# Kernel optimization log

Measured on AMD Instinct MI355X. Metric: run time of the kernel, lower is better.

Reference implementation:

```python
import jax, jax.numpy as jnp
import numpy as np

C = 64      # in_channels
H = 32      # hidden_size per direction
K = 8       # kernel_size
L = 4       # num_layers
EPS = 1e-5


def _sru_dir(x, W, v, b, reverse):
    # x: (T, N, in); one SRU direction.
    if reverse:
        x = x[::-1]
    U = x @ W                                   # (T, N, 4H): [candidate z, f_pre, r_pre, highway x']
    z, fp, rp, xp = jnp.split(U, 4, axis=-1)
    vf, vr = jnp.split(v, 2)
    bf, br = jnp.split(b, 2)

    def step(c, inp):
        z_t, fp_t, rp_t, xp_t = inp
        f = jax.nn.sigmoid(fp_t + vf * c + bf)
        r = jax.nn.sigmoid(rp_t + vr * c + br)
        c_new = f * c + (1.0 - f) * z_t
        h = r * c_new + (1.0 - r) * xp_t
        return c_new, h

    c0 = jnp.zeros((x.shape[1], H), x.dtype)
    _, h = jax.lax.scan(step, c0, (z, fp, rp, xp))
    if reverse:
        h = h[::-1]
    return h


def _sru(x, W0, Wr, v, b):
    # Bidirectional multi-layer SRU. x: (T, N, C*K) -> (T, N, 2H)
    Ws = [W0] + [Wr[i] for i in range(Wr.shape[0])]
    h = x
    for l in range(L):
        hf = _sru_dir(h, Ws[l][0], v[l, 0], b[l, 0], False)
        hb = _sru_dir(h, Ws[l][1], v[l, 1], b[l, 1], True)
        h = jnp.concatenate([hf, hb], axis=-1)
    return h


def setup_inputs() -> dict:
    key = jax.random.key(0)
    ks = jax.random.split(key, 8)
    B, Fdim, Tdim = 2, 128, 250
    s = 0.05
    x = jax.random.normal(ks[0], (B, C, Fdim, Tdim), jnp.float32)
    gamma = jnp.ones((C,), jnp.float32)
    beta = jnp.zeros((C,), jnp.float32)
    W0 = jax.random.normal(ks[1], (2, C * K, 4 * H), jnp.float32) * s       # layer 0, 2 dirs
    Wr = jax.random.normal(ks[2], (L - 1, 2, 2 * H, 4 * H), jnp.float32) * s  # layers 1..3
    v = jax.random.normal(ks[3], (L, 2, 2 * H), jnp.float32) * s            # recurrent gate vectors
    b = jnp.zeros((L, 2, 2 * H), jnp.float32)                               # gate biases
    wct = jax.random.normal(ks[4], (2 * H, C, K), jnp.float32) * s          # ConvTranspose1d (in,out,k)
    bct = jnp.zeros((C,), jnp.float32)
    return {"x": x, "gamma": gamma, "beta": beta, "W0": W0, "Wr": Wr,
            "v": v, "b": b, "wct": wct, "bct": bct}


def reference(x, gamma, beta, W0, Wr, v, b, wct, bct):
    x = jnp.swapaxes(x, -1, -2)                 # [B, C, T, F]
    res = x
    B, Cc, T, F = x.shape
    # GroupNorm(num_groups=1): normalize over (C,T,F) per sample, per-channel affine.
    mean = jnp.mean(x, axis=(1, 2, 3), keepdims=True)
    var = jnp.var(x, axis=(1, 2, 3), keepdims=True)
    xn = (x - mean) * jax.lax.rsqrt(var + EPS)
    xn = xn * gamma[None, :, None, None] + beta[None, :, None, None]
    # -> (B*F, C, T), then unfold over T with window K (channel-major block layout).
    xu = jnp.transpose(xn, (0, 3, 1, 2)).reshape(B * F, Cc, T)
    Tn = T - K + 1
    win = jnp.stack([xu[:, :, k:k + Tn] for k in range(K)], axis=2)   # (N, C, K, Tn)
    win = win.reshape(B * F, Cc * K, Tn)
    s = jnp.transpose(win, (2, 0, 1))           # (Tn, N, C*K)
    h = _sru(s, W0, Wr, v, b)                   # (Tn, N, 2H)
    y = jnp.transpose(h, (1, 2, 0))             # (N, 2H, Tn)
    # ConvTranspose1d stride 1 == full correlation with flipped kernel.
    w_conv = jnp.transpose(wct, (1, 0, 2))[:, :, ::-1]                # (out, in, k)
    y = jax.lax.conv_general_dilated(y, w_conv, (1,), [(K - 1, K - 1)],
                                     dimension_numbers=("NCH", "OIH", "NCH"))
    y = y + bct[None, :, None]                  # (N, C, T)
    y = y.reshape(B, F, Cc, T)
    y = jnp.transpose(y, (0, 2, 3, 1))          # [B, C, T, F]
    y = y + res
    return jnp.swapaxes(y, -1, -2)              # back to [B, C, F, T]
```

## Files before the change

kernel.cpp:

```cpp
#include <hip/hip_runtime.h>
#include <math.h>

#define Tt 250
#define TnN 243
#define Nn 256
#define EPS_ 1e-5f
#define LOG2E 1.44269504f

typedef unsigned short u16;
typedef __bf16 bf16x8 __attribute__((ext_vector_type(8)));
typedef float f32x4 __attribute__((ext_vector_type(4)));

__device__ __forceinline__ u16 f2bf(float f) {
    unsigned u = __builtin_bit_cast(unsigned, f);
    u += 0x7FFFu + ((u >> 16) & 1u);
    return (u16)(u >> 16);
}
__device__ __forceinline__ float bf2f(u16 s) {
    unsigned u = ((unsigned)s) << 16;
    return __builtin_bit_cast(float, u);
}
__device__ __forceinline__ float hw_exp2(float x) {
    return __builtin_amdgcn_exp2f(x);
}

__device__ __forceinline__ void async_load16(const void* g, void* l) {
    __builtin_amdgcn_global_load_lds(
        (const __attribute__((address_space(1))) unsigned int*)g,
        (__attribute__((address_space(3))) unsigned int*)l, 16, 0, 0);
}

__device__ __forceinline__ void dma72g(const u16* gsrc, int rstride, u16* ldst, int nseg,
                                       int w, int lane, int nw) {
    for (int seg = w; seg < nseg; seg += nw) {
        int c9 = seg * 64 + lane;
        int row = c9 / 9, sub = c9 - row * 9;
        const u16* src = (sub < 8) ? &gsrc[row * rstride + sub * 8] : gsrc;
        async_load16(src, ldst + seg * 512);
    }
}

template<int D>
__device__ __forceinline__ void chain_run(u16* Zr, u16* Fr, float kf, float bf_) {
    bf16x8 z8 = *(const bf16x8*)&Zr[D ? 240 : 0];
    bf16x8 f8 = *(const bf16x8*)&Fr[D ? 240 : 0];
    float c = 0.f;
    for (int grp = 0; grp < 31; ++grp) {
        int gb = D ? (30 - grp) * 8 : grp * 8;
        bf16x8 zn = z8, fn = f8;
        if (grp < 30) {
            int gbn = D ? (29 - grp) * 8 : (grp + 1) * 8;
            zn = *(const bf16x8*)&Zr[gbn];
            fn = *(const bf16x8*)&Fr[gbn];
        }
        bf16x8 co;
        #pragma unroll
        for (int k = 0; k < 8; ++k) {
            const int idx = D ? (7 - k) : k;
            int t = gb + idx;
            float uz = (float)z8[idx];
            float af = -LOG2E * ((float)f8[idx] + bf_);
            float xe = fmaf(kf, c, af);
            float fg = __builtin_amdgcn_rcpf(1.f + hw_exp2(xe));
            float cn = fmaf(fg, c - uz, uz);
            bool ok = (t < TnN);
            if (ok) c = cn;
            co[idx] = ok ? (__bf16)c : (__bf16)0.f;
        }
        *(bf16x8*)&Zr[gb] = co;
        z8 = zn; f8 = fn;
    }
}

__global__ __launch_bounds__(256) void k_stats(const float* __restrict__ x,
                                               float* __restrict__ stats) {
    __shared__ float ls[4], ls2[4];
    const int sb = blockIdx.x, tid = threadIdx.x;
    const int b = sb >> 7;
    const float4* xb = (const float4*)(x + (size_t)b * 64 * 128 * Tt);
    const int n4 = 64 * 128 * Tt / 4;
    float s = 0.f, s2 = 0.f;
    for (int i = (sb & 127) * 256 + tid; i < n4; i += 128 * 256) {
        float4 vv = xb[i];
        s  += vv.x + vv.y + vv.z + vv.w;
        s2 += vv.x * vv.x + vv.y * vv.y + vv.z * vv.z + vv.w * vv.w;
    }
    for (int off = 32; off; off >>= 1) {
        s  += __shfl_down(s, off);
        s2 += __shfl_down(s2, off);
    }
    int lane = tid & 63, w = tid >> 6;
    if (lane == 0) { ls[w] = s; ls2[w] = s2; }
    __syncthreads();
    if (tid == 0) {
        float a = 0.f, a2 = 0.f;
        for (int i = 0; i < 4; i++) { a += ls[i]; a2 += ls2[i]; }
        stats[sb * 2]     = a;
        stats[sb * 2 + 1] = a2;
    }
}

__global__ __launch_bounds__(512) void k_norm(const float* __restrict__ x, const float* __restrict__ stats,
                       const float* __restrict__ gamma, const float* __restrict__ beta,
                       const float* __restrict__ W0, const float* __restrict__ Wr,
                       const float* __restrict__ wct,
                       u16* __restrict__ xbt, u16* __restrict__ W0k,
                       u16* __restrict__ Wrt, u16* __restrict__ Wcto) {
    __shared__ u16 lt[64 * 260];
    __shared__ float sm2[2];
    const int n = blockIdx.x, tid = threadIdx.x;
    const int b = n >> 7, f = n & 127;
    if (tid < 64) {
        float a = 0.f, a2 = 0.f;
        #pragma unroll
        for (int p = 0; p < 2; ++p) {
            int sb = b * 128 + tid + p * 64;
            a  += stats[sb * 2];
            a2 += stats[sb * 2 + 1];
        }
        for (int off = 32; off; off >>= 1) {
            a  += __shfl_down(a, off);
            a2 += __shfl_down(a2, off);
        }
        if (tid == 0) { sm2[0] = a; sm2[1] = a2; }
    }
    #pragma unroll
    for (int it = 0; it < 2; ++it) {
        int idx = it * 131072 + n * 512 + tid;
        if (idx < 131072) {
            int k = idx >> 14, j = (idx >> 6) & 255, c = idx & 63;
            int d = j >> 7, ck = c * 8 + k;
            W0k[idx] = f2bf(W0[((size_t)d * 512 + ck) * 128 + (j & 127)]);
        } else if (idx < 180224) {
            int r = idx - 131072;
            int i = r & 63, j = (r >> 6) & 255, lidx = r >> 14;
            Wrt[r] = f2bf(Wr[(size_t)(lidx * 2 + (j >> 7)) * 8192 + i * 128 + (j & 127)]);
        } else if (idx < 212992) {
            int r = idx - 180224;
            int o = r >> 9; int k = r & 511; int kk = k >> 6, ci = k & 63;
            Wcto[r] = f2bf(wct[(size_t)ci * 512 + o * 8 + kk]);
        }
    }
    __syncthreads();
    const float inv = 1.0f / (float)(64 * 128 * Tt);
    float mean = sm2[0] * inv;
    float var  = sm2[1] * inv - mean * mean;
    float rstd = rsqrtf(var + EPS_);
    const int c = tid >> 3, vq = tid & 7;
    const float gm = gamma[c] * rstd;
    const float bt = beta[c] - mean * gm;
    const float* xr = x + ((size_t)(b * 64 + c) * 128 + f) * Tt;
    #pragma unroll
    for (int j = 0; j < 16; ++j) {
        int t0 = vq * 2 + j * 16;
        unsigned pv = 0u;
        if (t0 < Tt) {
            float2 xv = *(const float2*)&xr[t0];
            pv = (unsigned)f2bf(fmaf(xv.x, gm, bt)) | ((unsigned)f2bf(fmaf(xv.y, gm, bt)) << 16);
        }
        *(unsigned*)&lt[c * 260 + t0] = pv;
    }
    __syncthreads();
    const int cg = tid & 7, tq = tid >> 3;
    #pragma unroll
    for (int it = 0; it < 4; ++it) {
        int t = it * 64 + tq;
        u16 tmp[8];
        #pragma unroll
        for (int jj = 0; jj < 8; ++jj) tmp[jj] = lt[(cg * 8 + jj) * 260 + t];
        uint4 o;
        o.x = (unsigned)tmp[0] | ((unsigned)tmp[1] << 16);
        o.y = (unsigned)tmp[2] | ((unsigned)tmp[3] << 16);
        o.z = (unsigned)tmp[4] | ((unsigned)tmp[5] << 16);
        o.w = (unsigned)tmp[6] | ((unsigned)tmp[7] << 16);
        *(uint4*)&xbt[(size_t)n * 16384 + t * 64 + cg * 8] = o;
    }
}

#define HS0 0
#define ZT0 19008
#define FT0 34880
#define BM0 50752
#define SH_U16 81856
__global__ __launch_bounds__(1024) void k_tail(const u16* __restrict__ XbT,
                                               const u16* __restrict__ W0k,
                                               const u16* __restrict__ Wrt,
                                               const u16* __restrict__ Wc,
                                               const float* __restrict__ v,
                                               const float* __restrict__ bbias,
                                               const float* __restrict__ bct,
                                               const float* __restrict__ x,
                                               float* __restrict__ out) {
    __shared__ __align__(16) u16 sh[SH_U16];
    u16* Hs = sh + HS0;
    u16* ZT = sh + ZT0;
    u16* FT = sh + FT0;
    u16* Bm = sh + BM0;
    const int tid = threadIdx.x;
    const int n = blockIdx.x;
    const int lane = tid & 63, w = tid >> 6;
    const int ml = lane & 15, q = lane >> 4;
    const int wm = w >> 1, wn = w & 1;
    const int b = n >> 7, f = n & 127;

    for (int lay = 0; lay < 4; ++lay) {
        f32x4 acc[2][8];
        #pragma unroll
        for (int mt = 0; mt < 2; ++mt)
            #pragma unroll
            for (int nt = 0; nt < 8; ++nt) acc[mt][nt] = (f32x4){0.f, 0.f, 0.f, 0.f};

        if (lay == 0) {
            const u16* Xn = XbT + (size_t)n * 16384;
            u16* Bb0 = sh + ZT0;
            u16* Bb1 = Bm;
            dma72g(Xn, 64, Hs, 36, w, lane, 16);
            dma72g(W0k, 64, Bb0, 36, w, lane, 16);
            __syncthreads();
            #pragma unroll
            for (int k = 0; k < 8; ++k) {
                u16* Bl = (k & 1) ? Bb1 : Bb0;
                if (k < 7)
                    dma72g(W0k + (size_t)(k + 1) * 16384, 64, (k & 1) ? Bb0 : Bb1, 36, w, lane, 16);
                #pragma unroll
                for (int c2 = 0; c2 < 2; ++c2) {
                    int c0 = c2 * 32;
                    bf16x8 af[2];
                    #pragma unroll
                    for (int mt = 0; mt < 2; ++mt)
                        af[mt] = *(const bf16x8*)&Hs[(wm * 32 + mt * 16 + ml + k) * 72 + c0 + q * 8];
                    #pragma unroll
                    for (int nt = 0; nt < 8; ++nt) {
                        bf16x8 bfr = *(const bf16x8*)&Bl[(wn * 128 + nt * 16 + ml) * 72 + c0 + q * 8];
                        #pragma unroll
                        for (int mt = 0; mt < 2; ++mt)
                            acc[mt][nt] = __builtin_amdgcn_mfma_f32_16x16x32_bf16(af[mt], bfr, acc[mt][nt], 0, 0, 0);
                    }
                }
                __syncthreads();
            }
        } else {
            #pragma unroll
            for (int c2 = 0; c2 < 2; ++c2) {
                int c0 = c2 * 32;
                bf16x8 af[2];
                #pragma unroll
                for (int mt = 0; mt < 2; ++mt)
                    af[mt] = *(const bf16x8*)&Hs[(wm * 32 + mt * 16 + ml + 7) * 72 + c0 + q * 8];
                #pragma unroll
                for (int nt = 0; nt < 8; ++nt) {
                    bf16x8 bfr = *(const bf16x8*)&Bm[(wn * 128 + nt * 16 + ml) * 72 + c0 + q * 8];
                    #pragma unroll
                    for (int mt = 0; mt < 2; ++mt)
                        acc[mt][nt] = __builtin_amdgcn_mfma_f32_16x16x32_bf16(af[mt], bfr, acc[mt][nt], 0, 0, 0);
                }
            }
        }

        #pragma unroll
        for (int mt = 0; mt < 2; ++mt) {
            int t0 = wm * 32 + mt * 16 + q * 4;
            if (t0 < TnN) {
                bool vec = (t0 + 4 <= TnN);
                #pragma unroll
                for (int nt = 0; nt < 4; ++nt) {
                    int g2 = nt >> 1, hh = (nt & 1) * 16 + ml;
                    u16* P = (g2 ? FT : ZT) + (wn * 32 + hh) * 248;
                    if (vec) {
                        uint2 pv;
                        pv.x = (unsigned)f2bf(acc[mt][nt][0]) | ((unsigned)f2bf(acc[mt][nt][1]) << 16);
                        pv.y = (unsigned)f2bf(acc[mt][nt][2]) | ((unsigned)f2bf(acc[mt][nt][3]) << 16);
                        *(uint2*)&P[t0] = pv;
                    } else {
                        #pragma unroll
                        for (int r = 0; r < 4; ++r) {
                            int t = t0 + r;
                            if (t < TnN) P[t] = f2bf(acc[mt][nt][r]);
                        }
                    }
                }
            }
        }
        __syncthreads();

        if (lay < 3) {
            dma72g(Wrt + (size_t)lay * 16384, 64, Bm, 36, w, lane, 16);
        } else {
            #pragma unroll
            for (int i = 0; i < 4; ++i)
                dma72g(Wc + i * 64, 512, Bm + i * 4608, 9, w, lane, 16);
        }

        const float* vv = v + (size_t)(lay * 2) * 64;
        const float* bv = bbias + (size_t)(lay * 2) * 64;

        if (w < 2 && lane < 32) {
            const int d = w, h = lane;
            const float vf = vv[d * 64 + h], bf_ = bv[d * 64 + h];
            const float kf = -LOG2E * vf;
            u16* Zr = &ZT[(d * 32 + h) * 248];
            u16* Fr = &FT[(d * 32 + h) * 248];
            if (d == 0) chain_run<0>(Zr, Fr, kf, bf_);
            else        chain_run<1>(Zr, Fr, kf, bf_);
        }
        __syncthreads();

        if (lay == 0) {
            for (int i = tid; i < 21 * 72; i += 1024) {
                int r = i / 72, ci = i - r * 72;
                int row = r < 7 ? r : (TnN + r);
                Hs[row * 72 + ci] = 0;
            }
        }
        #pragma unroll
        for (int mt = 0; mt < 2; ++mt) {
            int t0 = wm * 32 + mt * 16 + q * 4;
            #pragma unroll
            for (int hi = 0; hi < 2; ++hi) {
                int hh = hi * 16 + ml;
                float vr_ = vv[wn * 64 + 32 + hh], br_ = bv[wn * 64 + 32 + hh];
                float kr = -LOG2E * vr_;
                const u16* Cr = &ZT[(wn * 32 + hh) * 248];
                f32x4 rp = acc[mt][4 + hi];
                f32x4 xp = acc[mt][6 + hi];
                #pragma unroll
                for (int r = 0; r < 4; ++r) {
                    int t = t0 + r;
                    if (t < TnN) {
                        float ct = bf2f(Cr[t]);
                        float cpr;
                        if (wn == 0) cpr = (t == 0) ? 0.f : bf2f(Cr[t - 1]);
                        else         cpr = (t == TnN - 1) ? 0.f : bf2f(Cr[t + 1]);
                        float xr = fmaf(kr, cpr, -LOG2E * (rp[r] + br_));
                        float rg = __builtin_amdgcn_rcpf(1.f + hw_exp2(xr));
                        float hv = fmaf(rg, ct - xp[r], xp[r]);
                        Hs[(t + 7) * 72 + wn * 32 + hh] = f2bf(hv);
                    }
                }
            }
        }
        __syncthreads();
    }

    {
        u16* T47 = sh + ZT0;
        float* Cf = (float*)(sh + 37440);
        const int tc0 = w * 16 + q * 4;
        f32x4 cacc[4] = {};
        #pragma unroll
        for (int i = 0; i < 4; ++i)
            dma72g(Wc + (4 + i) * 64, 512, T47 + i * 4608, 9, w, lane, 16);
        #pragma unroll
        for (int m = 0; m < 8; ++m) {
            if (m == 4) __syncthreads();
            const u16* Bl = (m < 4) ? (Bm + m * 4608) : (T47 + (m - 4) * 4608);
            #pragma unroll
            for (int c2 = 0; c2 < 2; ++c2) {
                int ci0 = c2 * 32;
                bf16x8 af = *(const bf16x8*)&Hs[(w * 16 + ml - m + 7) * 72 + ci0 + q * 8];
                #pragma unroll
                for (int nt = 0; nt < 4; ++nt) {
                    bf16x8 bfv = *(const bf16x8*)&Bl[(nt * 16 + ml) * 72 + ci0 + q * 8];
                    cacc[nt] = __builtin_amdgcn_mfma_f32_16x16x32_bf16(af, bfv, cacc[nt], 0, 0, 0);
                }
            }
        }
        __syncthreads();
        float bc[4];
        #pragma unroll
        for (int nt = 0; nt < 4; ++nt) bc[nt] = bct[nt * 16 + ml];
        #pragma unroll
        for (int r = 0; r < 4; ++r) {
            int t = tc0 + r;
            if (t < Tt) {
                #pragma unroll
                for (int nt = 0; nt < 4; ++nt)
                    Cf[t * 68 + nt * 16 + ml] = cacc[nt][r] + bc[nt];
            }
        }
        __syncthreads();
        {
            const int sub = tid & 15;
            const int o = tid >> 4;
            const float* xrow = x + ((size_t)(b * 64 + o) * 128 + f) * Tt;
            float* orow = out + ((size_t)(b * 64 + o) * 128 + f) * Tt;
            #pragma unroll
            for (int it = 0; it < 8; ++it) {
                int j = it * 32 + sub * 2;
                if (j < Tt) {
                    float2 xv = *(const float2*)&xrow[j];
                    float2 ov;
                    ov.x = Cf[j * 68 + o] + xv.x;
                    ov.y = Cf[(j + 1) * 68 + o] + xv.y;
                    *(float2*)&orow[j] = ov;
                }
            }
        }
    }
}

extern "C" void kernel_launch(void* const* d_in, const int* in_sizes, int n_in,
                              void* d_out, int out_size, void* d_ws, size_t ws_size,
                              hipStream_t stream) {
    (void)in_sizes; (void)n_in; (void)out_size; (void)ws_size;
    const float* x     = (const float*)d_in[0];
    const float* gamma = (const float*)d_in[1];
    const float* beta  = (const float*)d_in[2];
    const float* W0    = (const float*)d_in[3];
    const float* Wr    = (const float*)d_in[4];
    const float* v     = (const float*)d_in[5];
    const float* bb    = (const float*)d_in[6];
    const float* wct   = (const float*)d_in[7];
    const float* bct   = (const float*)d_in[8];
    float* out = (float*)d_out;

    char* base = (char*)d_ws;
    float* stats = (float*)base;
    u16* W0k  = (u16*)(base + 4096);
    u16* Wrt  = (u16*)(base + 4096 + 262144);
    u16* Wcto = (u16*)(base + 4096 + 262144 + 98304);
    u16* XbT  = (u16*)(base + 4096 + 262144 + 98304 + 65536);

    k_stats<<<dim3(256), 256, 0, stream>>>(x, stats);
    k_norm<<<dim3(256), 512, 0, stream>>>(x, stats, gamma, beta, W0, Wr, wct,
                                          XbT, W0k, Wrt, Wcto);
    k_tail<<<dim3(256), 1024, 0, stream>>>(XbT, W0k, Wrt, Wcto, v, bb, bct, x, out);
}
```

Baseline: 168.5 us.

## Fold normalization into layer-0 weights and merge stats with transpose pass

Moves the group-norm affine out of the activation path. gamma*rstd is folded into a per-batch copy of the layer-0 weights, and beta minus mean*gm is folded into a precomputed bias that initialises the accumulators. This lets the stats reduction and the input bf16 transpose run in one launch without waiting on each other. The ZT/FT row stride is padded from 248 to 252 and the r-gate pass uses vectorised bf16x4 loads of the cell state. The cost is a doubled W0 weight buffer, a serial 512-term dot loop per bias element, and rounding the unnormalized input to bf16 before scaling, which changes precision.

```diff
diff --git a/kernel.cpp b/kernel.cpp
--- a/kernel.cpp
+++ b/kernel.cpp
@@ -9,6 +9,7 @@
 
 typedef unsigned short u16;
 typedef __bf16 bf16x8 __attribute__((ext_vector_type(8)));
+typedef __bf16 bf16x4 __attribute__((ext_vector_type(4)));
 typedef float f32x4 __attribute__((ext_vector_type(4)));
 
 __device__ __forceinline__ u16 f2bf(float f) {
@@ -72,118 +73,143 @@
     }
 }
 
-__global__ __launch_bounds__(256) void k_stats(const float* __restrict__ x,
-                                               float* __restrict__ stats) {
-    __shared__ float ls[4], ls2[4];
-    const int sb = blockIdx.x, tid = threadIdx.x;
-    const int b = sb >> 7;
-    const float4* xb = (const float4*)(x + (size_t)b * 64 * 128 * Tt);
-    const int n4 = 64 * 128 * Tt / 4;
-    float s = 0.f, s2 = 0.f;
-    for (int i = (sb & 127) * 256 + tid; i < n4; i += 128 * 256) {
-        float4 vv = xb[i];
-        s  += vv.x + vv.y + vv.z + vv.w;
-        s2 += vv.x * vv.x + vv.y * vv.y + vv.z * vv.z + vv.w * vv.w;
-    }
-    for (int off = 32; off; off >>= 1) {
-        s  += __shfl_down(s, off);
-        s2 += __shfl_down(s2, off);
-    }
-    int lane = tid & 63, w = tid >> 6;
-    if (lane == 0) { ls[w] = s; ls2[w] = s2; }
-    __syncthreads();
-    if (tid == 0) {
-        float a = 0.f, a2 = 0.f;
-        for (int i = 0; i < 4; i++) { a += ls[i]; a2 += ls2[i]; }
-        stats[sb * 2]     = a;
-        stats[sb * 2 + 1] = a2;
-    }
-}
-
-__global__ __launch_bounds__(512) void k_norm(const float* __restrict__ x, const float* __restrict__ stats,
-                       const float* __restrict__ gamma, const float* __restrict__ beta,
-                       const float* __restrict__ W0, const float* __restrict__ Wr,
-                       const float* __restrict__ wct,
-                       u16* __restrict__ xbt, u16* __restrict__ W0k,
-                       u16* __restrict__ Wrt, u16* __restrict__ Wcto) {
-    __shared__ u16 lt[64 * 260];
-    __shared__ float sm2[2];
-    const int n = blockIdx.x, tid = threadIdx.x;
-    const int b = n >> 7, f = n & 127;
-    if (tid < 64) {
-        float a = 0.f, a2 = 0.f;
-        #pragma unroll
-        for (int p = 0; p < 2; ++p) {
-            int sb = b * 128 + tid + p * 64;
-            a  += stats[sb * 2];
-            a2 += stats[sb * 2 + 1];
-        }
+__global__ __launch_bounds__(512) void k_pre(const float* __restrict__ x,
+                                             float* __restrict__ stats,
+                                             u16* __restrict__ xbt) {
+    const int bx = blockIdx.x, tid = threadIdx.x;
+    if (bx < 256) {
+        __shared__ u16 lt[64 * 260];
+        const int n = bx;
+        const int b = n >> 7, f = n & 127;
+        const int c = tid >> 3, vq = tid & 7;
+        const float* xr = x + ((size_t)(b * 64 + c) * 128 + f) * Tt;
+        #pragma unroll
+        for (int j = 0; j < 16; ++j) {
+            int t0 = vq * 2 + j * 16;
+            unsigned pv = 0u;
+            if (t0 < Tt) {
+                float2 xv = *(const float2*)&xr[t0];
+                pv = (unsigned)f2bf(xv.x) | ((unsigned)f2bf(xv.y) << 16);
+            }
+            *(unsigned*)&lt[c * 260 + t0] = pv;
+        }
+        __syncthreads();
+        const int cg = tid & 7, tq = tid >> 3;
+        #pragma unroll
+        for (int it = 0; it < 4; ++it) {
+            int t = it * 64 + tq;
+            u16 tmp[8];
+            #pragma unroll
+            for (int jj = 0; jj < 8; ++jj) tmp[jj] = lt[(cg * 8 + jj) * 260 + t];
+            uint4 o;
+            o.x = (unsigned)tmp[0] | ((unsigned)tmp[1] << 16);
+            o.y = (unsigned)tmp[2] | ((unsigned)tmp[3] << 16);
+            o.z = (unsigned)tmp[4] | ((unsigned)tmp[5] << 16);
+            o.w = (unsigned)tmp[6] | ((unsigned)tmp[7] << 16);
+            *(uint4*)&xbt[(size_t)n * 16384 + t * 64 + cg * 8] = o;
+        }
+    } else {
+        __shared__ float ls[8], ls2[8];
+        const int sb = bx - 256;
+        const int b = sb >> 7;
+        const float4* xb = (const float4*)(x + (size_t)b * 64 * 128 * Tt);
+        const int n4 = 64 * 128 * Tt / 4;
+        float s = 0.f, s2 = 0.f;
+        for (int i = (sb & 127) * 512 + tid; i < n4; i += 128 * 512) {
+            float4 vv = xb[i];
+            s  += vv.x + vv.y + vv.z + vv.w;
+            s2 += vv.x * vv.x + vv.y * vv.y + vv.z * vv.z + vv.w * vv.w;
+        }
+        for (int off = 32; off; off >>= 1) {
+            s  += __shfl_down(s, off);
+            s2 += __shfl_down(s2, off);
+        }
+        int lane = tid & 63, w = tid >> 6;
+        if (lane == 0) { ls[w] = s; ls2[w] = s2; }
+        __syncthreads();
+        if (tid == 0) {
+            float a = 0.f, a2 = 0.f;
+            for (int i = 0; i < 8; i++) { a += ls[i]; a2 += ls2[i]; }
+            stats[sb * 2]     = a;
+            stats[sb * 2 + 1] = a2;
+        }
+    }
+}
+
+__global__ __launch_bounds__(512) void k_wpack(const float* __restrict__ stats,
+                                               const float* __restrict__ gamma,
+                                               const float* __restrict__ beta,
+                                               const float* __restrict__ W0,
+                                               const float* __restrict__ Wr,
+                                               const float* __restrict__ wct,
+                                               u16* __restrict__ W0kb,
+                                               u16* __restrict__ Wrt,
+                                               u16* __restrict__ Wcto,
+                                               float* __restrict__ bias0) {
+    __shared__ float ls[8], ls2[8], sm[4];
+    __shared__ float gm_s[128], bt_s[128];
+    const int bx = blockIdx.x, tid = threadIdx.x;
+    const float inv = 1.0f / (float)(64 * 128 * Tt);
+    if (tid < 256) {
+        float a = stats[tid * 2], a2 = stats[tid * 2 + 1];
         for (int off = 32; off; off >>= 1) {
             a  += __shfl_down(a, off);
             a2 += __shfl_down(a2, off);
         }
-        if (tid == 0) { sm2[0] = a; sm2[1] = a2; }
-    }
-    #pragma unroll
-    for (int it = 0; it < 2; ++it) {
-        int idx = it * 131072 + n * 512 + tid;
-        if (idx < 131072) {
-            int k = idx >> 14, j = (idx >> 6) & 255, c = idx & 63;
-            int d = j >> 7, ck = c * 8 + k;
-            W0k[idx] = f2bf(W0[((size_t)d * 512 + ck) * 128 + (j & 127)]);
-        } else if (idx < 180224) {
-            int r = idx - 131072;
-            int i = r & 63, j = (r >> 6) & 255, lidx = r >> 14;
-            Wrt[r] = f2bf(Wr[(size_t)(lidx * 2 + (j >> 7)) * 8192 + i * 128 + (j & 127)]);
-        } else if (idx < 212992) {
-            int r = idx - 180224;
-            int o = r >> 9; int k = r & 511; int kk = k >> 6, ci = k & 63;
-            Wcto[r] = f2bf(wct[(size_t)ci * 512 + o * 8 + kk]);
-        }
+        int lane = tid & 63, wv = tid >> 6;
+        if (lane == 0) { ls[wv] = a; ls2[wv] = a2; }
     }
     __syncthreads();
-    const float inv = 1.0f / (float)(64 * 128 * Tt);
-    float mean = sm2[0] * inv;
-    float var  = sm2[1] * inv - mean * mean;
-    float rstd = rsqrtf(var + EPS_);
-    const int c = tid >> 3, vq = tid & 7;
-    const float gm = gamma[c] * rstd;
-    const float bt = beta[c] - mean * gm;
-    const float* xr = x + ((size_t)(b * 64 + c) * 128 + f) * Tt;
-    #pragma unroll
-    for (int j = 0; j < 16; ++j) {
-        int t0 = vq * 2 + j * 16;
-        unsigned pv = 0u;
-        if (t0 < Tt) {
-            float2 xv = *(const float2*)&xr[t0];
-            pv = (unsigned)f2bf(fmaf(xv.x, gm, bt)) | ((unsigned)f2bf(fmaf(xv.y, gm, bt)) << 16);
-        }
-        *(unsigned*)&lt[c * 260 + t0] = pv;
+    if (tid < 2) {
+        float a  = ls[tid * 2] + ls[tid * 2 + 1];
+        float a2 = ls2[tid * 2] + ls2[tid * 2 + 1];
+        float mean = a * inv;
+        float var  = a2 * inv - mean * mean;
+        sm[tid * 2] = mean; sm[tid * 2 + 1] = rsqrtf(var + EPS_);
     }
     __syncthreads();
-    const int cg = tid & 7, tq = tid >> 3;
-    #pragma unroll
-    for (int it = 0; it < 4; ++it) {
-        int t = it * 64 + tq;
-        u16 tmp[8];
-        #pragma unroll
-        for (int jj = 0; jj < 8; ++jj) tmp[jj] = lt[(cg * 8 + jj) * 260 + t];
-        uint4 o;
-        o.x = (unsigned)tmp[0] | ((unsigned)tmp[1] << 16);
-        o.y = (unsigned)tmp[2] | ((unsigned)tmp[3] << 16);
-        o.z = (unsigned)tmp[4] | ((unsigned)tmp[5] << 16);
-        o.w = (unsigned)tmp[6] | ((unsigned)tmp[7] << 16);
-        *(uint4*)&xbt[(size_t)n * 16384 + t * 64 + cg * 8] = o;
+    if (tid < 128) {
+        int bb = tid >> 6, c = tid & 63;
+        float gm = gamma[c] * sm[bb * 2 + 1];
+        gm_s[tid] = gm;
+        bt_s[tid] = beta[c] - sm[bb * 2] * gm;
+    }
+    __syncthreads();
+
+    int idx = bx * 512 + tid;
+    if (idx < 262144) {
+        int b = idx >> 17, r = idx & 131071;
+        int k = r >> 14, j = (r >> 6) & 255, c = r & 63;
+        int d = j >> 7;
+        W0kb[idx] = f2bf(gm_s[b * 64 + c] * W0[((size_t)d * 512 + c * 8 + k) * 128 + (j & 127)]);
+    } else if (idx < 311296) {
+        int r = idx - 262144;
+        int i = r & 63, j = (r >> 6) & 255, lidx = r >> 14;
+        Wrt[r] = f2bf(Wr[(size_t)(lidx * 2 + (j >> 7)) * 8192 + i * 128 + (j & 127)]);
+    } else if (idx < 344064) {
+        int r = idx - 311296;
+        int o = r >> 9; int k = r & 511; int kk = k >> 6, ci = k & 63;
+        Wcto[r] = f2bf(wct[(size_t)ci * 512 + o * 8 + kk]);
+    } else if (idx < 344576) {
+        int r = idx - 344064;
+        int b = r >> 8, j = r & 255;
+        int d = j >> 7;
+        const float* W0d = W0 + (size_t)d * 512 * 128 + (j & 127);
+        float s = 0.f;
+        for (int ck = 0; ck < 512; ++ck)
+            s += bt_s[b * 64 + (ck >> 3)] * W0d[(size_t)ck * 128];
+        bias0[r] = s;
     }
 }
 
 #define HS0 0
 #define ZT0 19008
-#define FT0 34880
-#define BM0 50752
+#define FT0 35136
+#define BM0 51264
 #define SH_U16 81856
 __global__ __launch_bounds__(1024) void k_tail(const u16* __restrict__ XbT,
-                                               const u16* __restrict__ W0k,
+                                               const u16* __restrict__ W0kb,
+                                               const float* __restrict__ bias0,
                                                const u16* __restrict__ Wrt,
                                                const u16* __restrict__ Wc,
                                                const float* __restrict__ v,
@@ -205,23 +231,26 @@
 
     for (int lay = 0; lay < 4; ++lay) {
         f32x4 acc[2][8];
-        #pragma unroll
-        for (int mt = 0; mt < 2; ++mt)
-            #pragma unroll
-            for (int nt = 0; nt < 8; ++nt) acc[mt][nt] = (f32x4){0.f, 0.f, 0.f, 0.f};
 
         if (lay == 0) {
+            #pragma unroll
+            for (int nt = 0; nt < 8; ++nt) {
+                float bv0 = bias0[b * 256 + wn * 128 + nt * 16 + ml];
+                acc[0][nt] = (f32x4){bv0, bv0, bv0, bv0};
+                acc[1][nt] = acc[0][nt];
+            }
             const u16* Xn = XbT + (size_t)n * 16384;
+            const u16* W0n = W0kb + (size_t)b * 131072;
             u16* Bb0 = sh + ZT0;
             u16* Bb1 = Bm;
             dma72g(Xn, 64, Hs, 36, w, lane, 16);
-            dma72g(W0k, 64, Bb0, 36, w, lane, 16);
+            dma72g(W0n, 64, Bb0, 36, w, lane, 16);
             __syncthreads();
             #pragma unroll
             for (int k = 0; k < 8; ++k) {
                 u16* Bl = (k & 1) ? Bb1 : Bb0;
                 if (k < 7)
-                    dma72g(W0k + (size_t)(k + 1) * 16384, 64, (k & 1) ? Bb0 : Bb1, 36, w, lane, 16);
+                    dma72g(W0n + (size_t)(k + 1) * 16384, 64, (k & 1) ? Bb0 : Bb1, 36, w, lane, 16);
                 #pragma unroll
                 for (int c2 = 0; c2 < 2; ++c2) {
                     int c0 = c2 * 32;
@@ -241,6 +270,10 @@
             }
         } else {
             #pragma unroll
+            for (int mt = 0; mt < 2; ++mt)
+                #pragma unroll
+                for (int nt = 0; nt < 8; ++nt) acc[mt][nt] = (f32x4){0.f, 0.f, 0.f, 0.f};
+            #pragma unroll
             for (int c2 = 0; c2 < 2; ++c2) {
                 int c0 = c2 * 32;
                 bf16x8 af[2];
@@ -265,7 +298,7 @@
                 #pragma unroll
                 for (int nt = 0; nt < 4; ++nt) {
                     int g2 = nt >> 1, hh = (nt & 1) * 16 + ml;
-                    u16* P = (g2 ? FT : ZT) + (wn * 32 + hh) * 248;
+                    u16* P = (g2 ? FT : ZT) + (wn * 32 + hh) * 252;
                     if (vec) {
                         uint2 pv;
                         pv.x = (unsigned)f2bf(acc[mt][nt][0]) | ((unsigned)f2bf(acc[mt][nt][1]) << 16);
@@ -298,8 +331,8 @@
             const int d = w, h = lane;
             const float vf = vv[d * 64 + h], bf_ = bv[d * 64 + h];
             const float kf = -LOG2E * vf;
-            u16* Zr = &ZT[(d * 32 + h) * 248];
-            u16* Fr = &FT[(d * 32 + h) * 248];
+            u16* Zr = &ZT[(d * 32 + h) * 252];
+            u16* Fr = &FT[(d * 32 + h) * 252];
             if (d == 0) chain_run<0>(Zr, Fr, kf, bf_);
             else        chain_run<1>(Zr, Fr, kf, bf_);
         }
@@ -315,26 +348,38 @@
         #pragma unroll
         for (int mt = 0; mt < 2; ++mt) {
             int t0 = wm * 32 + mt * 16 + q * 4;
-            #pragma unroll
-            for (int hi = 0; hi < 2; ++hi) {
-                int hh = hi * 16 + ml;
-                float vr_ = vv[wn * 64 + 32 + hh], br_ = bv[wn * 64 + 32 + hh];
-                float kr = -LOG2E * vr_;
-                const u16* Cr = &ZT[(wn * 32 + hh) * 248];
-                f32x4 rp = acc[mt][4 + hi];
-                f32x4 xp = acc[mt][6 + hi];
-                #pragma unroll
-                for (int r = 0; r < 4; ++r) {
-                    int t = t0 + r;
-                    if (t < TnN) {
-                        float ct = bf2f(Cr[t]);
-                        float cpr;
-                        if (wn == 0) cpr = (t == 0) ? 0.f : bf2f(Cr[t - 1]);
-                        else         cpr = (t == TnN - 1) ? 0.f : bf2f(Cr[t + 1]);
-                        float xr = fmaf(kr, cpr, -LOG2E * (rp[r] + br_));
-                        float rg = __builtin_amdgcn_rcpf(1.f + hw_exp2(xr));
-                        float hv = fmaf(rg, ct - xp[r], xp[r]);
-                        Hs[(t + 7) * 72 + wn * 32 + hh] = f2bf(hv);
+            if (t0 < TnN) {
+                #pragma unroll
+                for (int hi = 0; hi < 2; ++hi) {
+                    int hh = hi * 16 + ml;
+                    float vr_ = vv[wn * 64 + 32 + hh], br_ = bv[wn * 64 + 32 + hh];
+                    float kr = -LOG2E * vr_;
+                    const u16* Cr = &ZT[(wn * 32 + hh) * 252];
+                    bf16x4 c4 = *(const bf16x4*)&Cr[t0];
+                    float ct[4];
+                    #pragma unroll
+                    for (int r = 0; r < 4; ++r) ct[r] = (float)c4[r];
+                    float cprv[4];
+                    if (wn == 0) {
+                        cprv[0] = (t0 == 0) ? 0.f : bf2f(Cr[t0 - 1]);
+                        cprv[1] = ct[0]; cprv[2] = ct[1]; cprv[3] = ct[2];
+                    } else {
+                        cprv[0] = ct[1]; cprv[1] = ct[2]; cprv[2] = ct[3];
+                        cprv[3] = bf2f(Cr[t0 + 4]);
+                    }
+                    f32x4 rp = acc[mt][4 + hi];
+                    f32x4 xp = acc[mt][6 + hi];
+                    #pragma unroll
+                    for (int r = 0; r < 4; ++r) {
+                        int t = t0 + r;
+                        if (t < TnN) {
+                            float cpr = cprv[r];
+                            if (wn == 1 && t == TnN - 1) cpr = 0.f;
+                            float xr = fmaf(kr, cpr, -LOG2E * (rp[r] + br_));
+                            float rg = __builtin_amdgcn_rcpf(1.f + hw_exp2(xr));
+                            float hv = fmaf(rg, ct[r] - xp[r], xp[r]);
+                            Hs[(t + 7) * 72 + wn * 32 + hh] = f2bf(hv);
+                        }
                     }
                 }
             }
@@ -416,13 +461,14 @@
 
     char* base = (char*)d_ws;
     float* stats = (float*)base;
-    u16* W0k  = (u16*)(base + 4096);
-    u16* Wrt  = (u16*)(base + 4096 + 262144);
-    u16* Wcto = (u16*)(base + 4096 + 262144 + 98304);
-    u16* XbT  = (u16*)(base + 4096 + 262144 + 98304 + 65536);
-
-    k_stats<<<dim3(256), 256, 0, stream>>>(x, stats);
-    k_norm<<<dim3(256), 512, 0, stream>>>(x, stats, gamma, beta, W0, Wr, wct,
-                                          XbT, W0k, Wrt, Wcto);
-    k_tail<<<dim3(256), 1024, 0, stream>>>(XbT, W0k, Wrt, Wcto, v, bb, bct, x, out);
-}
+    float* bias0 = (float*)(base + 2048);
+    u16* W0kb = (u16*)(base + 4096);
+    u16* Wrt  = (u16*)(base + 4096 + 524288);
+    u16* Wcto = (u16*)(base + 4096 + 524288 + 98304);
+    u16* XbT  = (u16*)(base + 4096 + 524288 + 98304 + 65536);
+
+    k_pre<<<dim3(512), 512, 0, stream>>>(x, stats, XbT);
+    k_wpack<<<dim3(673), 512, 0, stream>>>(stats, gamma, beta, W0, Wr, wct,
+                                           W0kb, Wrt, Wcto, bias0);
+    k_tail<<<dim3(256), 1024, 0, stream>>>(XbT, W0kb, bias0, Wrt, Wcto, v, bb, bct, x, out);
+}
```

Result: slower. 187.2 us (+11.1%).
